# Kernel tuning notes

Measured on AMD Instinct MI355X. Metric: run time of the kernel, lower is better.

The kernel has to match this reference:

```python
import jax, jax.numpy as jnp
import numpy as np

N, E = 50000, 800000
IN_F, HID, NCLS, NLAYERS = 64, 64, 2, 3
BN_EPS = 1e-5


def batch_norm(x, gamma, beta):
    # training-mode BatchNorm1d: biased batch statistics over the node/edge dim
    m = jnp.mean(x, axis=0)
    v = jnp.var(x, axis=0)
    return gamma * (x - m) * jax.lax.rsqrt(v + BN_EPS) + beta


def setup_inputs() -> dict:
    key = jax.random.key(0)
    ks = jax.random.split(key, 24)
    L, Lp1 = NLAYERS, NLAYERS + 1

    def lin(k, fan_in, shape):
        bound = 1.0 / np.sqrt(fan_in)
        return jax.random.uniform(k, shape, jnp.float32, -bound, bound)

    return {
        "h": jax.random.normal(ks[0], (N, IN_F), jnp.float32),
        "src": jax.random.randint(ks[1], (E,), 0, N, jnp.int32),
        "dst": jax.random.randint(ks[2], (E,), 0, N, jnp.int32),
        "emb_W": lin(ks[3], IN_F, (IN_F, HID)),
        "emb_b": lin(ks[4], IN_F, (HID,)),
        "mlp_W1": lin(ks[5], HID, (L, HID, HID)),
        "mlp_b1": lin(ks[6], HID, (L, HID)),
        "mlp_bn_g": jnp.ones((L, HID), jnp.float32),
        "mlp_bn_b": jnp.zeros((L, HID), jnp.float32),
        "mlp_W2": lin(ks[7], HID, (L, HID, HID)),
        "mlp_b2": lin(ks[8], HID, (L, HID)),
        "apply_bn_g": jnp.ones((L, HID), jnp.float32),
        "apply_bn_b": jnp.zeros((L, HID), jnp.float32),
        "out_bn_g": jnp.ones((L, HID), jnp.float32),
        "out_bn_b": jnp.zeros((L, HID), jnp.float32),
        "pred_W1": lin(ks[9], 2 * HID, (Lp1, 2 * HID, HID)),
        "pred_b1": lin(ks[10], 2 * HID, (Lp1, HID)),
        "pred_W2": lin(ks[11], HID, (Lp1, HID, NCLS)),
        "pred_b2": lin(ks[12], HID, (Lp1, NCLS)),
    }


def reference(h, src, dst, emb_W, emb_b, mlp_W1, mlp_b1, mlp_bn_g, mlp_bn_b,
              mlp_W2, mlp_b2, apply_bn_g, apply_bn_b, out_bn_g, out_bn_b,
              pred_W1, pred_b1, pred_W2, pred_b2):
    n_layers = mlp_W1.shape[0]
    n_nodes = h.shape[0]

    def edge_feat(hn):
        # concat src and dst node features per edge -> [E, 2*HID]
        return jnp.concatenate([hn[src], hn[dst]], axis=1)

    hn = h @ emb_W + emb_b  # embedding_h
    edge_reps = [edge_feat(hn)]

    for i in range(n_layers):
        # GINConv (sum aggregation, eps=0): (1+eps)*h_v + sum_{u->v} h_u
        agg = jax.ops.segment_sum(hn[src], dst, num_segments=n_nodes)
        z = hn + agg
        # MLP (depth 2): Linear -> BN -> ReLU -> Linear
        z = jax.nn.relu(batch_norm(z @ mlp_W1[i] + mlp_b1[i], mlp_bn_g[i], mlp_bn_b[i]))
        z = z @ mlp_W2[i] + mlp_b2[i]
        # ApplyNodeFunc: BN + ReLU
        z = jax.nn.relu(batch_norm(z, apply_bn_g[i], apply_bn_b[i]))
        # outer per-layer BN + ReLU
        hn = jax.nn.relu(batch_norm(z, out_bn_g[i], out_bn_b[i]))
        edge_reps.append(edge_feat(hn))

    # sum of per-layer edge predictions: Linear(2h->h) -> ReLU -> Linear(h->ncls)
    score = jnp.zeros((src.shape[0], pred_W2.shape[-1]), h.dtype)
    for i, e in enumerate(edge_reps):
        score = score + jax.nn.relu(e @ pred_W1[i] + pred_b1[i]) @ pred_W2[i] + pred_b2[i]
    return score
```

## Files before the change

### kernel.cpp

```cpp
#include <hip/hip_runtime.h>
#include <hip/hip_bf16.h>


#define BN_EPS 1e-5f

__global__ __launch_bounds__(256) void hist_kernel(const int* __restrict__ dst,
                                                   int* __restrict__ deg, int E) {
  int i = blockIdx.x * blockDim.x + threadIdx.x;
  int stride = gridDim.x * blockDim.x;
  for (; i < E; i += stride) atomicAdd(&deg[dst[i]], 1);
}

__global__ __launch_bounds__(256) void scan1_kernel(const int* __restrict__ deg,
                                                    int* __restrict__ rowstart,
                                                    int* __restrict__ partials, int N) {
  __shared__ int wsum[4];
  int tid = threadIdx.x;
  int lane = tid & 63, w = tid >> 6;
  int base = blockIdx.x * 1024 + tid * 4;
  int d0 = 0, d1 = 0, d2 = 0, d3 = 0;
  if (base + 3 < N) {
    int4 v = *reinterpret_cast<const int4*>(deg + base);
    d0 = v.x; d1 = v.y; d2 = v.z; d3 = v.w;
  } else {
    if (base + 0 < N) d0 = deg[base + 0];
    if (base + 1 < N) d1 = deg[base + 1];
    if (base + 2 < N) d2 = deg[base + 2];
  }
  int t0 = d0, t1 = t0 + d1, t2 = t1 + d2, t3 = t2 + d3;
  int tot = t3;
  int inc = tot;
#pragma unroll
  for (int off = 1; off < 64; off <<= 1) {
    int v = __shfl_up(inc, off);
    if (lane >= off) inc += v;
  }
  if (lane == 63) wsum[w] = inc;
  __syncthreads();
  int woff = 0;
  for (int k = 0; k < w; ++k) woff += wsum[k];
  int excl = woff + inc - tot;
  if (base + 0 < N) rowstart[base + 0] = excl;
  if (base + 1 < N) rowstart[base + 1] = excl + t0;
  if (base + 2 < N) rowstart[base + 2] = excl + t1;
  if (base + 3 < N) rowstart[base + 3] = excl + t2;
  if (tid == 255) partials[blockIdx.x] = excl + t3;
}

__global__ __launch_bounds__(64) void scan2_kernel(int* __restrict__ partials,
                                                   int* __restrict__ rowstart_end,
                                                   int NB) {
  int lane = threadIdx.x;
  int v = (lane < NB) ? partials[lane] : 0;
  int inc = v;
#pragma unroll
  for (int off = 1; off < 64; off <<= 1) {
    int t = __shfl_up(inc, off);
    if (lane >= off) inc += t;
  }
  if (lane < NB) partials[lane] = inc - v;
  if (lane == 63) *rowstart_end = inc;
}

__global__ __launch_bounds__(256) void scan3_kernel(const int* __restrict__ partials,
                                                    int* __restrict__ rowstart,
                                                    int* __restrict__ cursor, int N) {
  int off = partials[blockIdx.x];
  int base = blockIdx.x * 1024 + threadIdx.x * 4;
#pragma unroll
  for (int k = 0; k < 4; ++k) {
    int i = base + k;
    if (i < N) {
      int r = rowstart[i] + off;
      rowstart[i] = r;
      cursor[i] = r;
    }
  }
}

__global__ __launch_bounds__(256) void fill_kernel(const int* __restrict__ src,
                                                   const int* __restrict__ dst,
                                                   int* __restrict__ cursor,
                                                   int* __restrict__ eidx, int E) {
  int i = blockIdx.x * blockDim.x + threadIdx.x;
  int stride = gridDim.x * blockDim.x;
  for (; i < E; i += stride) {
    int p = atomicAdd(&cursor[dst[i]], 1);
    eidx[p] = src[i];
  }
}

__global__ __launch_bounds__(256) void agg_kernel(const float* __restrict__ hn,
                                                  const ushort* __restrict__ hnb,
                                                  const int* __restrict__ rowstart,
                                                  const int* __restrict__ eidx,
                                                  float* __restrict__ z, int N) {
  int lane = threadIdx.x & 63;
  int v = blockIdx.x * 4 + (threadIdx.x >> 6);
  if (v >= N) return;
  float acc = hn[(size_t)v * 64 + lane];
  int p0 = rowstart[v], p1 = rowstart[v + 1];
  for (int p = p0; p < p1; ++p) {
    int u = eidx[p];
    acc += __uint_as_float(((unsigned)hnb[(size_t)u * 64 + lane]) << 16);
  }
  z[(size_t)v * 64 + lane] = acc;
}

__global__ __launch_bounds__(256) void gemm64_kernel(
    const float* __restrict__ in, const float* __restrict__ W,
    const float* __restrict__ bias, const float* __restrict__ stats_in,
    const float* __restrict__ g_in, const float* __restrict__ b_in,
    float* __restrict__ out, float* __restrict__ stats_out,
    __hip_bfloat16* __restrict__ out_bf, int N) {
  __shared__ float sW[64][64];
  __shared__ float sx[32][64];
  __shared__ float red[2][4][64];
  int tid = threadIdx.x;
  int lane = tid & 63, w = tid >> 6;
  int n0 = blockIdx.x * 32;
#pragma unroll
  for (int r = 0; r < 16; ++r) {
    int idx = r * 256 + tid;
    sW[idx >> 6][idx & 63] = W[idx];
  }
  float sc = 1.f, sh = 0.f;
  if (stats_in) {
    float invN = 1.0f / (float)N;
    float m = stats_in[lane] * invN;
    float var = stats_in[64 + lane] * invN - m * m;
    sc = g_in[lane] * rsqrtf(var + BN_EPS);
    sh = b_in[lane] - m * sc;
  }
#pragma unroll
  for (int r = 0; r < 8; ++r) {
    int idx = r * 256 + tid;
    int n = n0 + (idx >> 6);
    float x = (n < N) ? in[(size_t)n * 64 + lane] : 0.f;
    if (stats_in) x = fmaxf(x * sc + sh, 0.f);
    sx[idx >> 6][lane] = x;
  }
  __syncthreads();
  float acc[8];
  float bz = bias ? bias[lane] : 0.f;
#pragma unroll
  for (int j = 0; j < 8; ++j) acc[j] = bz;
  for (int k = 0; k < 64; ++k) {
    float wv = sW[k][lane];
#pragma unroll
    for (int j = 0; j < 8; ++j) acc[j] = fmaf(sx[w * 8 + j][k], wv, acc[j]);
  }
  float ps = 0.f, pq = 0.f;
#pragma unroll
  for (int j = 0; j < 8; ++j) {
    int n = n0 + w * 8 + j;
    if (n < N) {
      out[(size_t)n * 64 + lane] = acc[j];
      if (out_bf) out_bf[(size_t)n * 64 + lane] = __float2bfloat16(acc[j]);
      ps += acc[j];
      pq += acc[j] * acc[j];
    }
  }
  if (stats_out) {
    red[0][w][lane] = ps;
    red[1][w][lane] = pq;
    __syncthreads();
    if (w == 0) {
      float s = red[0][0][lane] + red[0][1][lane] + red[0][2][lane] + red[0][3][lane];
      float q = red[1][0][lane] + red[1][1][lane] + red[1][2][lane] + red[1][3][lane];
      atomicAdd(&stats_out[lane], s);
      atomicAdd(&stats_out[64 + lane], q);
    }
  }
}

__global__ __launch_bounds__(256) void proj_kernel(const float* __restrict__ hn,
                                                   const float* __restrict__ W1,
                                                   const float* __restrict__ b1,
                                                   __hip_bfloat16* __restrict__ P1,
                                                   __hip_bfloat16* __restrict__ P2,
                                                   int N) {
  __shared__ float sWa[64][64];
  __shared__ float sWb[64][64];
  __shared__ float sx[32][64];
  int tid = threadIdx.x, lane = tid & 63, w = tid >> 6;
  int n0 = blockIdx.x * 32;
#pragma unroll
  for (int r = 0; r < 16; ++r) {
    int idx = r * 256 + tid;
    sWa[idx >> 6][idx & 63] = W1[idx];
    sWb[idx >> 6][idx & 63] = W1[4096 + idx];
  }
#pragma unroll
  for (int r = 0; r < 8; ++r) {
    int idx = r * 256 + tid;
    int n = n0 + (idx >> 6);
    sx[idx >> 6][lane] = (n < N) ? hn[(size_t)n * 64 + lane] : 0.f;
  }
  __syncthreads();
  float a1[8], a2[8];
  float bz = b1[lane];
#pragma unroll
  for (int j = 0; j < 8; ++j) { a1[j] = bz; a2[j] = 0.f; }
  for (int k = 0; k < 64; ++k) {
    float wa = sWa[k][lane];
    float wb = sWb[k][lane];
#pragma unroll
    for (int j = 0; j < 8; ++j) {
      float x = sx[w * 8 + j][k];
      a1[j] = fmaf(x, wa, a1[j]);
      a2[j] = fmaf(x, wb, a2[j]);
    }
  }
#pragma unroll
  for (int j = 0; j < 8; ++j) {
    int n = n0 + w * 8 + j;
    if (n < N) {
      P1[(size_t)n * 64 + lane] = __float2bfloat16(a1[j]);
      P2[(size_t)n * 64 + lane] = __float2bfloat16(a2[j]);
    }
  }
}

__global__ __launch_bounds__(256) void bnrelu_kernel(
    const float* __restrict__ in, const float* __restrict__ stats_in,
    const float* __restrict__ g_in, const float* __restrict__ b_in,
    float* __restrict__ out, float* __restrict__ stats_out,
    __hip_bfloat16* __restrict__ out_bf, int N) {
  __shared__ float red[2][4][64];
  int tid = threadIdx.x;
  int lane = tid & 63, w = tid >> 6;
  float invN = 1.0f / (float)N;
  float m = stats_in[lane] * invN;
  float var = stats_in[64 + lane] * invN - m * m;
  float sc = g_in[lane] * rsqrtf(var + BN_EPS);
  float sh = b_in[lane] - m * sc;
  float ps = 0.f, pq = 0.f;
  int rows_per_grid = gridDim.x * (blockDim.x >> 6);
  for (int n = blockIdx.x * (blockDim.x >> 6) + w; n < N; n += rows_per_grid) {
    float x = fmaxf(in[(size_t)n * 64 + lane] * sc + sh, 0.f);
    out[(size_t)n * 64 + lane] = x;
    if (out_bf) out_bf[(size_t)n * 64 + lane] = __float2bfloat16(x);
    ps += x;
    pq += x * x;
  }
  if (stats_out) {
    red[0][w][lane] = ps;
    red[1][w][lane] = pq;
    __syncthreads();
    if (w == 0) {
      float s = red[0][0][lane] + red[0][1][lane] + red[0][2][lane] + red[0][3][lane];
      float q = red[1][0][lane] + red[1][1][lane] + red[1][2][lane] + red[1][3][lane];
      atomicAdd(&stats_out[lane], s);
      atomicAdd(&stats_out[64 + lane], q);
    }
  }
}

__global__ __launch_bounds__(256) void edge_score_kernel(
    const ushort* __restrict__ P1, const ushort* __restrict__ P2,
    const int* __restrict__ src, const int* __restrict__ dst,
    const float* __restrict__ W2, const float* __restrict__ b2,
    float* __restrict__ out, int E, int first) {
  __shared__ float sW2[128];
  int tid = threadIdx.x;
  if (tid < 128) sW2[tid] = W2[tid];
  __syncthreads();
  int t = blockIdx.x * blockDim.x + tid;
  int e = t >> 3;
  if (e >= E) return;
  int sub = t & 7;
  int s = src[e], d = dst[e];
  uint4 ua = *reinterpret_cast<const uint4*>(P1 + (size_t)s * 64 + sub * 8);
  uint4 ub = *reinterpret_cast<const uint4*>(P2 + (size_t)d * 64 + sub * 8);
  unsigned av[4] = {ua.x, ua.y, ua.z, ua.w};
  unsigned bv[4] = {ub.x, ub.y, ub.z, ub.w};
  const float* w = sW2 + sub * 16;
  float p0 = 0.f, p1 = 0.f;
#pragma unroll
  for (int k = 0; k < 4; ++k) {
    float a_lo = __uint_as_float(av[k] << 16);
    float a_hi = __uint_as_float(av[k] & 0xffff0000u);
    float b_lo = __uint_as_float(bv[k] << 16);
    float b_hi = __uint_as_float(bv[k] & 0xffff0000u);
    float v0 = fmaxf(a_lo + b_lo, 0.f);
    float v1 = fmaxf(a_hi + b_hi, 0.f);
    p0 = fmaf(v0, w[4 * k + 0], fmaf(v1, w[4 * k + 2], p0));
    p1 = fmaf(v0, w[4 * k + 1], fmaf(v1, w[4 * k + 3], p1));
  }
#pragma unroll
  for (int mm = 1; mm < 8; mm <<= 1) {
    p0 += __shfl_xor(p0, mm);
    p1 += __shfl_xor(p1, mm);
  }
  if (sub == 0) {
    float o0 = p0 + b2[0];
    float o1 = p1 + b2[1];
    if (!first) {
      o0 += out[(size_t)e * 2];
      o1 += out[(size_t)e * 2 + 1];
    }
    out[(size_t)e * 2] = o0;
    out[(size_t)e * 2 + 1] = o1;
  }
}

extern "C" void kernel_launch(void* const* d_in, const int* in_sizes, int n_in,
                              void* d_out, int out_size, void* d_ws, size_t ws_size,
                              hipStream_t stream) {
  const float* h          = (const float*)d_in[0];
  const int*   src        = (const int*)d_in[1];
  const int*   dst        = (const int*)d_in[2];
  const float* emb_W      = (const float*)d_in[3];
  const float* emb_b      = (const float*)d_in[4];
  const float* mlp_W1     = (const float*)d_in[5];
  const float* mlp_b1     = (const float*)d_in[6];
  const float* mlp_bn_g   = (const float*)d_in[7];
  const float* mlp_bn_b   = (const float*)d_in[8];
  const float* mlp_W2     = (const float*)d_in[9];
  const float* mlp_b2     = (const float*)d_in[10];
  const float* apply_bn_g = (const float*)d_in[11];
  const float* apply_bn_b = (const float*)d_in[12];
  const float* out_bn_g   = (const float*)d_in[13];
  const float* out_bn_b   = (const float*)d_in[14];
  const float* pred_W1    = (const float*)d_in[15];
  const float* pred_b1    = (const float*)d_in[16];
  const float* pred_W2    = (const float*)d_in[17];
  const float* pred_b2    = (const float*)d_in[18];

  const int N = in_sizes[0] / 64;
  const int E = in_sizes[1];
  const size_t NF = (size_t)N * 64;
  const int NB1 = (N + 1023) / 1024;

  float* ws = (float*)d_ws;
  float* hn = ws;
  float* zb = hn + NF;
  float* z1 = zb + NF;
  float* z2 = z1 + NF;
  __hip_bfloat16* hnb = (__hip_bfloat16*)(z2 + NF);
  __hip_bfloat16* P1  = hnb + NF;
  __hip_bfloat16* P2  = P1 + NF;
  int* eidx     = (int*)(P2 + NF);
  int* rowstart = eidx + E;
  int* cursor   = rowstart + (N + 64);
  int* partials = cursor + (N + 64);
  int* deg      = partials + 64;
  float* stats  = (float*)(deg + (N + 64));

  size_t need = (size_t)((char*)(stats + 9 * 128) - (char*)d_ws);
  if (need > ws_size) return;

  hipMemsetAsync(deg, 0, ((size_t)(N + 64) + 9 * 128) * sizeof(int), stream);

  const int gemmBlocks = (N + 31) / 32;
  const int edgeBlocks = (int)(((size_t)E * 8 + 255) / 256);

  gemm64_kernel<<<gemmBlocks, 256, 0, stream>>>(h, emb_W, emb_b, nullptr, nullptr,
                                                nullptr, hn, nullptr, hnb, N);
  hist_kernel<<<1024, 256, 0, stream>>>(dst, deg, E);
  scan1_kernel<<<NB1, 256, 0, stream>>>(deg, rowstart, partials, N);
  scan2_kernel<<<1, 64, 0, stream>>>(partials, rowstart + N, NB1);
  scan3_kernel<<<NB1, 256, 0, stream>>>(partials, rowstart, cursor, N);
  fill_kernel<<<1024, 256, 0, stream>>>(src, dst, cursor, eidx, E);

  proj_kernel<<<gemmBlocks, 256, 0, stream>>>(hn, pred_W1, pred_b1, P1, P2, N);
  edge_score_kernel<<<edgeBlocks, 256, 0, stream>>>((const ushort*)P1, (const ushort*)P2,
                                                    src, dst, pred_W2, pred_b2,
                                                    (float*)d_out, E, 1);

  for (int i = 0; i < 3; ++i) {
    float* st1 = stats + (size_t)(3 * i + 0) * 128;
    float* st2 = stats + (size_t)(3 * i + 1) * 128;
    float* st3 = stats + (size_t)(3 * i + 2) * 128;
    agg_kernel<<<(N + 3) / 4, 256, 0, stream>>>(hn, (const ushort*)hnb, rowstart,
                                                eidx, zb, N);
    gemm64_kernel<<<gemmBlocks, 256, 0, stream>>>(zb, mlp_W1 + (size_t)i * 4096,
                                                  mlp_b1 + i * 64, nullptr, nullptr,
                                                  nullptr, z1, st1, nullptr, N);
    gemm64_kernel<<<gemmBlocks, 256, 0, stream>>>(z1, mlp_W2 + (size_t)i * 4096,
                                                  mlp_b2 + i * 64, st1,
                                                  mlp_bn_g + i * 64, mlp_bn_b + i * 64,
                                                  z2, st2, nullptr, N);
    bnrelu_kernel<<<784, 256, 0, stream>>>(z2, st2, apply_bn_g + i * 64,
                                           apply_bn_b + i * 64, z1, st3, nullptr, N);
    bnrelu_kernel<<<784, 256, 0, stream>>>(z1, st3, out_bn_g + i * 64,
                                           out_bn_b + i * 64, hn, nullptr, hnb, N);
    proj_kernel<<<gemmBlocks, 256, 0, stream>>>(hn, pred_W1 + (size_t)(i + 1) * 8192,
                                                pred_b1 + (i + 1) * 64, P1, P2, N);
    edge_score_kernel<<<edgeBlocks, 256, 0, stream>>>((const ushort*)P1, (const ushort*)P2,
                                                      src, dst,
                                                      pred_W2 + (i + 1) * 128,
                                                      pred_b2 + (i + 1) * 2,
                                                      (float*)d_out, E, 0);
  }
}
```

Before: 1.034 ms.

## Fuse outer BN+ReLU into consumers and score edges via dst-sorted CSR

Removes the second bnrelu pass per layer by applying the outer BatchNorm+ReLU on the fly inside the aggregation kernel and the projection kernel, using the stored batch statistics. The edge scoring kernel now walks edges in dst-sorted CSR order, loading P2 once per destination node and scattering results back through a new edge-order permutation array. The aggregation loop is unrolled by 8 to keep more gathers in flight. In exchange, BN+ReLU is recomputed per gathered neighbour, the final output writes become scattered, and the bf16 copy now holds pre-BN values.

```diff
diff --git a/kernel.cpp b/kernel.cpp
--- a/kernel.cpp
+++ b/kernel.cpp
@@ -3,6 +3,10 @@
 
 
 #define BN_EPS 1e-5f
+
+static __device__ __forceinline__ float bf2f(ushort u) {
+  return __uint_as_float(((unsigned)u) << 16);
+}
 
 __global__ __launch_bounds__(256) void hist_kernel(const int* __restrict__ dst,
                                                    int* __restrict__ deg, int E) {
@@ -81,28 +85,61 @@
 __global__ __launch_bounds__(256) void fill_kernel(const int* __restrict__ src,
                                                    const int* __restrict__ dst,
                                                    int* __restrict__ cursor,
-                                                   int* __restrict__ eidx, int E) {
+                                                   int* __restrict__ eidx,
+                                                   int* __restrict__ eord, int E) {
   int i = blockIdx.x * blockDim.x + threadIdx.x;
   int stride = gridDim.x * blockDim.x;
   for (; i < E; i += stride) {
     int p = atomicAdd(&cursor[dst[i]], 1);
     eidx[p] = src[i];
-  }
-}
-
-__global__ __launch_bounds__(256) void agg_kernel(const float* __restrict__ hn,
-                                                  const ushort* __restrict__ hnb,
-                                                  const int* __restrict__ rowstart,
-                                                  const int* __restrict__ eidx,
-                                                  float* __restrict__ z, int N) {
+    eord[p] = i;
+  }
+}
+
+template <int TR>
+__global__ __launch_bounds__(256) void agg_kernel(
+    const float* __restrict__ c, const ushort* __restrict__ cb,
+    const int* __restrict__ rowstart, const int* __restrict__ eidx,
+    const float* __restrict__ stats_in, const float* __restrict__ g_in,
+    const float* __restrict__ b_in, float* __restrict__ z, int N) {
   int lane = threadIdx.x & 63;
   int v = blockIdx.x * 4 + (threadIdx.x >> 6);
   if (v >= N) return;
-  float acc = hn[(size_t)v * 64 + lane];
-  int p0 = rowstart[v], p1 = rowstart[v + 1];
-  for (int p = p0; p < p1; ++p) {
-    int u = eidx[p];
-    acc += __uint_as_float(((unsigned)hnb[(size_t)u * 64 + lane]) << 16);
+  float sc = 1.f, sh = 0.f;
+  if (TR) {
+    float invN = 1.0f / (float)N;
+    float m = stats_in[lane] * invN;
+    float var = stats_in[64 + lane] * invN - m * m;
+    sc = g_in[lane] * rsqrtf(var + BN_EPS);
+    sh = b_in[lane] - m * sc;
+  }
+  float x0 = c[(size_t)v * 64 + lane];
+  float acc = TR ? fmaxf(x0 * sc + sh, 0.f) : x0;
+  int p = rowstart[v], pe = rowstart[v + 1];
+  for (; p + 8 <= pe; p += 8) {
+    int u[8];
+#pragma unroll
+    for (int k = 0; k < 8; ++k) u[k] = eidx[p + k];
+    float x[8];
+#pragma unroll
+    for (int k = 0; k < 8; ++k) x[k] = bf2f(cb[(size_t)u[k] * 64 + lane]);
+#pragma unroll
+    for (int k = 0; k < 8; ++k) acc += TR ? fmaxf(x[k] * sc + sh, 0.f) : x[k];
+  }
+  if (p + 4 <= pe) {
+    int u[4];
+#pragma unroll
+    for (int k = 0; k < 4; ++k) u[k] = eidx[p + k];
+#pragma unroll
+    for (int k = 0; k < 4; ++k) {
+      float x = bf2f(cb[(size_t)u[k] * 64 + lane]);
+      acc += TR ? fmaxf(x * sc + sh, 0.f) : x;
+    }
+    p += 4;
+  }
+  for (; p < pe; ++p) {
+    float x = bf2f(cb[(size_t)eidx[p] * 64 + lane]);
+    acc += TR ? fmaxf(x * sc + sh, 0.f) : x;
   }
   z[(size_t)v * 64 + lane] = acc;
 }
@@ -174,12 +211,11 @@
   }
 }
 
-__global__ __launch_bounds__(256) void proj_kernel(const float* __restrict__ hn,
-                                                   const float* __restrict__ W1,
-                                                   const float* __restrict__ b1,
-                                                   __hip_bfloat16* __restrict__ P1,
-                                                   __hip_bfloat16* __restrict__ P2,
-                                                   int N) {
+__global__ __launch_bounds__(256) void proj_kernel(
+    const float* __restrict__ c, const float* __restrict__ W1,
+    const float* __restrict__ b1, const float* __restrict__ stats_in,
+    const float* __restrict__ g_in, const float* __restrict__ b_in,
+    __hip_bfloat16* __restrict__ P1, __hip_bfloat16* __restrict__ P2, int N) {
   __shared__ float sWa[64][64];
   __shared__ float sWb[64][64];
   __shared__ float sx[32][64];
@@ -191,11 +227,21 @@
     sWa[idx >> 6][idx & 63] = W1[idx];
     sWb[idx >> 6][idx & 63] = W1[4096 + idx];
   }
+  float sc = 1.f, sh = 0.f;
+  if (stats_in) {
+    float invN = 1.0f / (float)N;
+    float m = stats_in[lane] * invN;
+    float var = stats_in[64 + lane] * invN - m * m;
+    sc = g_in[lane] * rsqrtf(var + BN_EPS);
+    sh = b_in[lane] - m * sc;
+  }
 #pragma unroll
   for (int r = 0; r < 8; ++r) {
     int idx = r * 256 + tid;
     int n = n0 + (idx >> 6);
-    sx[idx >> 6][lane] = (n < N) ? hn[(size_t)n * 64 + lane] : 0.f;
+    float x = (n < N) ? c[(size_t)n * 64 + lane] : 0.f;
+    if (stats_in) x = fmaxf(x * sc + sh, 0.f);
+    sx[idx >> 6][lane] = x;
   }
   __syncthreads();
   float a1[8], a2[8];
@@ -257,51 +303,58 @@
   }
 }
 
-__global__ __launch_bounds__(256) void edge_score_kernel(
+__global__ __launch_bounds__(256) void edge_score_csr_kernel(
     const ushort* __restrict__ P1, const ushort* __restrict__ P2,
-    const int* __restrict__ src, const int* __restrict__ dst,
-    const float* __restrict__ W2, const float* __restrict__ b2,
-    float* __restrict__ out, int E, int first) {
-  __shared__ float sW2[128];
-  int tid = threadIdx.x;
-  if (tid < 128) sW2[tid] = W2[tid];
-  __syncthreads();
-  int t = blockIdx.x * blockDim.x + tid;
-  int e = t >> 3;
-  if (e >= E) return;
-  int sub = t & 7;
-  int s = src[e], d = dst[e];
-  uint4 ua = *reinterpret_cast<const uint4*>(P1 + (size_t)s * 64 + sub * 8);
-  uint4 ub = *reinterpret_cast<const uint4*>(P2 + (size_t)d * 64 + sub * 8);
-  unsigned av[4] = {ua.x, ua.y, ua.z, ua.w};
-  unsigned bv[4] = {ub.x, ub.y, ub.z, ub.w};
-  const float* w = sW2 + sub * 16;
-  float p0 = 0.f, p1 = 0.f;
+    const int* __restrict__ rowstart, const int* __restrict__ eidx,
+    const int* __restrict__ eord, const float* __restrict__ W2,
+    const float* __restrict__ b2, float* __restrict__ out, int N, int first) {
+  int lane = threadIdx.x & 63;
+  int v = blockIdx.x * 4 + (threadIdx.x >> 6);
+  if (v >= N) return;
+  int sub = lane & 7;
+  int grp = lane >> 3;
+  float w[16];
+  const float4* wp = reinterpret_cast<const float4*>(W2 + sub * 16);
 #pragma unroll
   for (int k = 0; k < 4; ++k) {
-    float a_lo = __uint_as_float(av[k] << 16);
-    float a_hi = __uint_as_float(av[k] & 0xffff0000u);
-    float b_lo = __uint_as_float(bv[k] << 16);
-    float b_hi = __uint_as_float(bv[k] & 0xffff0000u);
-    float v0 = fmaxf(a_lo + b_lo, 0.f);
-    float v1 = fmaxf(a_hi + b_hi, 0.f);
-    p0 = fmaf(v0, w[4 * k + 0], fmaf(v1, w[4 * k + 2], p0));
-    p1 = fmaf(v0, w[4 * k + 1], fmaf(v1, w[4 * k + 3], p1));
-  }
-#pragma unroll
-  for (int mm = 1; mm < 8; mm <<= 1) {
-    p0 += __shfl_xor(p0, mm);
-    p1 += __shfl_xor(p1, mm);
-  }
-  if (sub == 0) {
-    float o0 = p0 + b2[0];
-    float o1 = p1 + b2[1];
-    if (!first) {
-      o0 += out[(size_t)e * 2];
-      o1 += out[(size_t)e * 2 + 1];
-    }
-    out[(size_t)e * 2] = o0;
-    out[(size_t)e * 2 + 1] = o1;
+    float4 t = wp[k];
+    w[4 * k + 0] = t.x; w[4 * k + 1] = t.y; w[4 * k + 2] = t.z; w[4 * k + 3] = t.w;
+  }
+  float bb0 = b2[0], bb1 = b2[1];
+  uint4 pb = *reinterpret_cast<const uint4*>(P2 + (size_t)v * 64 + sub * 8);
+  unsigned bv[4] = {pb.x, pb.y, pb.z, pb.w};
+  int p0 = rowstart[v], p1 = rowstart[v + 1];
+  for (int p = p0 + grp; p < p1; p += 8) {
+    int s = eidx[p];
+    int e = eord[p];
+    uint4 pa = *reinterpret_cast<const uint4*>(P1 + (size_t)s * 64 + sub * 8);
+    unsigned av[4] = {pa.x, pa.y, pa.z, pa.w};
+    float q0 = 0.f, q1 = 0.f;
+#pragma unroll
+    for (int k = 0; k < 4; ++k) {
+      float a_lo = __uint_as_float(av[k] << 16);
+      float a_hi = __uint_as_float(av[k] & 0xffff0000u);
+      float b_lo = __uint_as_float(bv[k] << 16);
+      float b_hi = __uint_as_float(bv[k] & 0xffff0000u);
+      float v0 = fmaxf(a_lo + b_lo, 0.f);
+      float v1 = fmaxf(a_hi + b_hi, 0.f);
+      q0 = fmaf(v0, w[4 * k + 0], fmaf(v1, w[4 * k + 2], q0));
+      q1 = fmaf(v0, w[4 * k + 1], fmaf(v1, w[4 * k + 3], q1));
+    }
+#pragma unroll
+    for (int mm = 1; mm < 8; mm <<= 1) {
+      q0 += __shfl_xor(q0, mm);
+      q1 += __shfl_xor(q1, mm);
+    }
+    if (sub == 0) {
+      float o0 = q0 + bb0, o1 = q1 + bb1;
+      if (!first) {
+        o0 += out[(size_t)e * 2];
+        o1 += out[(size_t)e * 2 + 1];
+      }
+      out[(size_t)e * 2] = o0;
+      out[(size_t)e * 2 + 1] = o1;
+    }
   }
 }
 
@@ -334,15 +387,16 @@
   const int NB1 = (N + 1023) / 1024;
 
   float* ws = (float*)d_ws;
-  float* hn = ws;
-  float* zb = hn + NF;
+  float* c  = ws;
+  float* zb = c + NF;
   float* z1 = zb + NF;
   float* z2 = z1 + NF;
-  __hip_bfloat16* hnb = (__hip_bfloat16*)(z2 + NF);
-  __hip_bfloat16* P1  = hnb + NF;
-  __hip_bfloat16* P2  = P1 + NF;
+  __hip_bfloat16* cb = (__hip_bfloat16*)(z2 + NF);
+  __hip_bfloat16* P1 = cb + NF;
+  __hip_bfloat16* P2 = P1 + NF;
   int* eidx     = (int*)(P2 + NF);
-  int* rowstart = eidx + E;
+  int* eord     = eidx + E;
+  int* rowstart = eord + E;
   int* cursor   = rowstart + (N + 64);
   int* partials = cursor + (N + 64);
   int* deg      = partials + 64;
@@ -354,27 +408,37 @@
   hipMemsetAsync(deg, 0, ((size_t)(N + 64) + 9 * 128) * sizeof(int), stream);
 
   const int gemmBlocks = (N + 31) / 32;
-  const int edgeBlocks = (int)(((size_t)E * 8 + 255) / 256);
+  const int nodeBlocks = (N + 3) / 4;
 
   gemm64_kernel<<<gemmBlocks, 256, 0, stream>>>(h, emb_W, emb_b, nullptr, nullptr,
-                                                nullptr, hn, nullptr, hnb, N);
+                                                nullptr, c, nullptr, cb, N);
   hist_kernel<<<1024, 256, 0, stream>>>(dst, deg, E);
   scan1_kernel<<<NB1, 256, 0, stream>>>(deg, rowstart, partials, N);
   scan2_kernel<<<1, 64, 0, stream>>>(partials, rowstart + N, NB1);
   scan3_kernel<<<NB1, 256, 0, stream>>>(partials, rowstart, cursor, N);
-  fill_kernel<<<1024, 256, 0, stream>>>(src, dst, cursor, eidx, E);
-
-  proj_kernel<<<gemmBlocks, 256, 0, stream>>>(hn, pred_W1, pred_b1, P1, P2, N);
-  edge_score_kernel<<<edgeBlocks, 256, 0, stream>>>((const ushort*)P1, (const ushort*)P2,
-                                                    src, dst, pred_W2, pred_b2,
-                                                    (float*)d_out, E, 1);
+  fill_kernel<<<1024, 256, 0, stream>>>(src, dst, cursor, eidx, eord, E);
+
+  proj_kernel<<<gemmBlocks, 256, 0, stream>>>(c, pred_W1, pred_b1, nullptr, nullptr,
+                                              nullptr, P1, P2, N);
+  edge_score_csr_kernel<<<nodeBlocks, 256, 0, stream>>>(
+      (const ushort*)P1, (const ushort*)P2, rowstart, eidx, eord, pred_W2, pred_b2,
+      (float*)d_out, N, 1);
 
   for (int i = 0; i < 3; ++i) {
     float* st1 = stats + (size_t)(3 * i + 0) * 128;
     float* st2 = stats + (size_t)(3 * i + 1) * 128;
     float* st3 = stats + (size_t)(3 * i + 2) * 128;
-    agg_kernel<<<(N + 3) / 4, 256, 0, stream>>>(hn, (const ushort*)hnb, rowstart,
-                                                eidx, zb, N);
+    const float* stP = (i == 0) ? nullptr : stats + (size_t)(3 * (i - 1) + 2) * 128;
+    const float* gP  = (i == 0) ? nullptr : out_bn_g + (i - 1) * 64;
+    const float* bP  = (i == 0) ? nullptr : out_bn_b + (i - 1) * 64;
+
+    if (i == 0)
+      agg_kernel<0><<<nodeBlocks, 256, 0, stream>>>(c, (const ushort*)cb, rowstart,
+                                                    eidx, nullptr, nullptr, nullptr,
+                                                    zb, N);
+    else
+      agg_kernel<1><<<nodeBlocks, 256, 0, stream>>>(c, (const ushort*)cb, rowstart,
+                                                    eidx, stP, gP, bP, zb, N);
     gemm64_kernel<<<gemmBlocks, 256, 0, stream>>>(zb, mlp_W1 + (size_t)i * 4096,
                                                   mlp_b1 + i * 64, nullptr, nullptr,
                                                   nullptr, z1, st1, nullptr, N);
@@ -383,15 +447,13 @@
                                                   mlp_bn_g + i * 64, mlp_bn_b + i * 64,
                                                   z2, st2, nullptr, N);
     bnrelu_kernel<<<784, 256, 0, stream>>>(z2, st2, apply_bn_g + i * 64,
-                                           apply_bn_b + i * 64, z1, st3, nullptr, N);
-    bnrelu_kernel<<<784, 256, 0, stream>>>(z1, st3, out_bn_g + i * 64,
-                                           out_bn_b + i * 64, hn, nullptr, hnb, N);
-    proj_kernel<<<gemmBlocks, 256, 0, stream>>>(hn, pred_W1 + (size_t)(i + 1) * 8192,
-                                                pred_b1 + (i + 1) * 64, P1, P2, N);
-    edge_score_kernel<<<edgeBlocks, 256, 0, stream>>>((const ushort*)P1, (const ushort*)P2,
-                                                      src, dst,
-                                                      pred_W2 + (i + 1) * 128,
-                                                      pred_b2 + (i + 1) * 2,
-                                                      (float*)d_out, E, 0);
-  }
-}
+                                           apply_bn_b + i * 64, c, st3, cb, N);
+    proj_kernel<<<gemmBlocks, 256, 0, stream>>>(c, pred_W1 + (size_t)(i + 1) * 8192,
+                                                pred_b1 + (i + 1) * 64, st3,
+                                                out_bn_g + i * 64, out_bn_b + i * 64,
+                                                P1, P2, N);
+    edge_score_csr_kernel<<<nodeBlocks, 256, 0, stream>>>(
+        (const ushort*)P1, (const ushort*)P2, rowstart, eidx, eord,
+        pred_W2 + (i + 1) * 128, pred_b2 + (i + 1) * 2, (float*)d_out, N, 0);
+  }
+}
```

Measured after the change: 928.1 us. 1.11x faster.
